# Kernel tuning notes

Measured on AMD Instinct MI355X. Metric: run time of the kernel, lower is better.

The kernel has to match this reference:

```python
import jax, jax.numpy as jnp
import numpy as np

N_NODES = 50000
N_EDGES = 800000
D = 64
N_GRAPHS = 500  # 100 nodes per graph


def setup_inputs() -> dict:
    key = jax.random.key(0)
    k1, k2, k3, k4, k5, k6 = jax.random.split(key, 6)
    x = jax.random.normal(k1, (N_NODES, D), dtype=jnp.float32)
    edge_index = jax.random.randint(k2, (2, N_EDGES), 0, N_NODES, dtype=jnp.int32)
    split_n = jnp.full((N_GRAPHS,), N_NODES // N_GRAPHS, dtype=jnp.int32)
    # edge_att_mlp: Linear(2*D, 1)
    W_edge = jax.random.normal(k3, (2 * D, 1), dtype=jnp.float32) * 0.05
    b_edge = jax.random.normal(k4, (1,), dtype=jnp.float32) * 0.05
    # node_att_cov: GCNConv(D, 1)
    W_gcn = jax.random.normal(k5, (D, 1), dtype=jnp.float32) * 0.05
    b_gcn = jax.random.normal(k6, (1,), dtype=jnp.float32) * 0.05
    return {"x": x, "edge_index": edge_index, "split_n": split_n,
            "W_edge": W_edge, "b_edge": b_edge, "W_gcn": W_gcn, "b_gcn": b_gcn}


def _segment_softmax(v, seg, num_segments):
    # softmax over dim 0 within each segment (replaces lazy_soft's python loop)
    m = jax.ops.segment_max(v, seg, num_segments=num_segments)
    e = jnp.exp(v - m[seg])
    s = jax.ops.segment_sum(e, seg, num_segments=num_segments)
    return e / s[seg]


def reference(x, edge_index, split_n, W_edge, b_edge, W_gcn, b_gcn):
    n = x.shape[0]
    row, col = edge_index[0], edge_index[1]

    # edge attention: gather pair, linear, sigmoid
    edge_rep = jnp.concatenate([x[row], x[col]], axis=-1)  # [E, 2D]
    edge_att = jax.nn.sigmoid(edge_rep @ W_edge + b_edge)  # [E, 1]
    edge_att_m = edge_att
    edge_att_s = 1.0 - edge_att

    # GCNConv(D, 1): add self-loops, symmetric deg^-1/2 norm, linear, scatter-sum
    h = x @ W_gcn  # [N, 1]
    loop = jnp.arange(n, dtype=row.dtype)
    src = jnp.concatenate([row, loop])
    dst = jnp.concatenate([col, loop])
    deg = jnp.zeros((n,), dtype=x.dtype).at[dst].add(1.0)
    dinv = jax.lax.rsqrt(deg)  # deg >= 1 due to self-loops
    norm = dinv[src] * dinv[dst]  # [E+N]
    node_att = jax.ops.segment_sum(norm[:, None] * h[src], dst, num_segments=n) + b_gcn

    # per-graph ragged softmax (fused segment softmax)
    seg = jnp.repeat(jnp.arange(split_n.shape[0]), split_n, total_repeat_length=n)
    node_att_m = _segment_softmax(node_att, seg, split_n.shape[0])
    node_att_s = _segment_softmax(1.0 - node_att_m, seg, split_n.shape[0])
    return edge_att_m, edge_att_s, node_att_m, node_att_s
```

## Files before the change

kernel.cpp:

```cpp
#include <hip/hip_runtime.h>
#include <math.h>


#define RANGE 8192
#define BD_H 1024
#define SOFT_LDS_CAP 2048

__global__ __launch_bounds__(BD_H)
void k1_node_hist(const float* __restrict__ x,
                  const float* __restrict__ W_edge,
                  const float* __restrict__ W_gcn,
                  const int* __restrict__ ei,
                  float2* __restrict__ ed2,
                  float* __restrict__ hbuf,
                  float* __restrict__ partial,
                  int N, int E, int C, int R, int CH, int nodeBlocks, int vec) {
    __shared__ float table[RANGE];
    const int bid = blockIdx.x, tid = threadIdx.x;
    if (bid < nodeBlocks) {
        float4* Wsh = (float4*)table;
        if (tid < 32) Wsh[tid] = ((const float4*)W_edge)[tid];
        else if (tid < 48) Wsh[tid] = ((const float4*)W_gcn)[tid - 32];
        __syncthreads();
        int lane = tid & 15;
        long long gid = (long long)bid * BD_H + tid;
        int i = (int)(gid >> 4);
        if (i >= N) return;
        float4 v = ((const float4*)(x + (size_t)i * 64))[lane];
        float4 wa = Wsh[lane], wb = Wsh[16 + lane], wg = Wsh[32 + lane];
        float p1 = v.x*wa.x + v.y*wa.y + v.z*wa.z + v.w*wa.w;
        float p2 = v.x*wb.x + v.y*wb.y + v.z*wb.z + v.w*wb.w;
        float p3 = v.x*wg.x + v.y*wg.y + v.z*wg.z + v.w*wg.w;
#pragma unroll
        for (int s = 1; s < 16; s <<= 1) {
            p1 += __shfl_xor(p1, s);
            p2 += __shfl_xor(p2, s);
            p3 += __shfl_xor(p3, s);
        }
        if (lane == 0) {
            ed2[i] = make_float2(p1, p2);
            hbuf[i] = p3;
        }
        return;
    }
    const int hb = bid - nodeBlocks;
    const int c = hb / R;
    const int r = hb - c * R;
    const int lo = r * RANGE;
    for (int j = tid; j < RANGE; j += BD_H) table[j] = 0.f;
    __syncthreads();
    const int e_lo = c * CH;
    const int e_hi = (E < e_lo + CH) ? E : (e_lo + CH);
    const int* __restrict__ col = ei + E;
    for (int e = e_lo + tid * 4; e < e_hi; e += BD_H * 4) {
        if (vec && e + 3 < e_hi) {
            int4 cc = *(const int4*)(col + e);
            unsigned u;
            u = (unsigned)(cc.x - lo); if (u < RANGE) atomicAdd(&table[u], 1.f);
            u = (unsigned)(cc.y - lo); if (u < RANGE) atomicAdd(&table[u], 1.f);
            u = (unsigned)(cc.z - lo); if (u < RANGE) atomicAdd(&table[u], 1.f);
            u = (unsigned)(cc.w - lo); if (u < RANGE) atomicAdd(&table[u], 1.f);
        } else {
            int ee = (e_hi < e + 4) ? e_hi : e + 4;
            for (int q = e; q < ee; ++q) {
                unsigned u = (unsigned)(col[q] - lo);
                if (u < RANGE) atomicAdd(&table[u], 1.f);
            }
        }
    }
    __syncthreads();
    const size_t base = (size_t)c * N;
    for (int j = tid; j < RANGE; j += BD_H) {
        int node = lo + j;
        if (node < N) partial[base + node] = table[j];
    }
}

__global__ __launch_bounds__(256)
void k2_dinv_sig(const int* __restrict__ ei,
                 const float2* __restrict__ ed2,
                 const float* __restrict__ b_edge,
                 const float* __restrict__ partial,
                 float* __restrict__ hbuf,
                 float* __restrict__ dv1,
                 float* __restrict__ om, float* __restrict__ os,
                 int N, int E, int C, int dinvBlocks, int vec) {
    const int bid = blockIdx.x, tid = threadIdx.x;
    if (bid < dinvBlocks) {
        int i = bid * 256 + tid;
        if (i >= N) return;
        float d0 = 1.f, d1 = 0.f, d2 = 0.f, d3 = 0.f;
        int c = 0;
        for (; c + 3 < C; c += 4) {
            d0 += partial[(size_t)(c + 0) * N + i];
            d1 += partial[(size_t)(c + 1) * N + i];
            d2 += partial[(size_t)(c + 2) * N + i];
            d3 += partial[(size_t)(c + 3) * N + i];
        }
        for (; c < C; ++c) d0 += partial[(size_t)c * N + i];
        float dv = rsqrtf((d0 + d1) + (d2 + d3));
        hbuf[i] *= dv;
        dv1[i] = dv;
        return;
    }
    int t = (bid - dinvBlocks) * 256 + tid;
    int e0 = t * 4;
    const float b = b_edge[0];
    if (vec && e0 + 3 < E) {
        int4 r = *(const int4*)(ei + e0);
        int4 c = *(const int4*)(ei + E + e0);
        float4 m;
        m.x = 1.f / (1.f + expf(-(ed2[r.x].x + ed2[c.x].y + b)));
        m.y = 1.f / (1.f + expf(-(ed2[r.y].x + ed2[c.y].y + b)));
        m.z = 1.f / (1.f + expf(-(ed2[r.z].x + ed2[c.z].y + b)));
        m.w = 1.f / (1.f + expf(-(ed2[r.w].x + ed2[c.w].y + b)));
        *(float4*)(om + e0) = m;
        *(float4*)(os + e0) = make_float4(1.f - m.x, 1.f - m.y, 1.f - m.z, 1.f - m.w);
    } else if (e0 < E) {
        int ee = (E < e0 + 4) ? E : e0 + 4;
        for (int e = e0; e < ee; ++e) {
            float a = 1.f / (1.f + expf(-(ed2[ei[e]].x + ed2[ei[E + e]].y + b)));
            om[e] = a; os[e] = 1.f - a;
        }
    }
}

__global__ __launch_bounds__(BD_H)
void k3_scat(const int* __restrict__ ei,
             const float* __restrict__ g1,
             float* __restrict__ partial,
             int N, int E, int C, int R, int CH, int vec) {
    __shared__ float table[RANGE];
    const int tid = threadIdx.x;
    const int c = blockIdx.x / R;
    const int r = blockIdx.x - c * R;
    const int lo = r * RANGE;
    for (int j = tid; j < RANGE; j += BD_H) table[j] = 0.f;
    __syncthreads();
    const int e_lo = c * CH;
    const int e_hi = (E < e_lo + CH) ? E : (e_lo + CH);
    const int* __restrict__ row = ei;
    const int* __restrict__ col = ei + E;
    for (int e = e_lo + tid * 4; e < e_hi; e += BD_H * 4) {
        if (vec && e + 3 < e_hi) {
            int4 cc = *(const int4*)(col + e);
            int4 rr = *(const int4*)(row + e);
            unsigned u;
            u = (unsigned)(cc.x - lo); if (u < RANGE) atomicAdd(&table[u], g1[rr.x]);
            u = (unsigned)(cc.y - lo); if (u < RANGE) atomicAdd(&table[u], g1[rr.y]);
            u = (unsigned)(cc.z - lo); if (u < RANGE) atomicAdd(&table[u], g1[rr.z]);
            u = (unsigned)(cc.w - lo); if (u < RANGE) atomicAdd(&table[u], g1[rr.w]);
        } else {
            int ee = (e_hi < e + 4) ? e_hi : e + 4;
            for (int q = e; q < ee; ++q) {
                unsigned u = (unsigned)(col[q] - lo);
                if (u < RANGE) atomicAdd(&table[u], g1[row[q]]);
            }
        }
    }
    __syncthreads();
    const size_t base = (size_t)c * N;
    for (int j = tid; j < RANGE; j += BD_H) {
        int node = lo + j;
        if (node < N) partial[base + node] = table[j];
    }
}

__global__ __launch_bounds__(128)
void k4_softmax(const float* __restrict__ hbuf,
                const float* __restrict__ dv1,
                const float* __restrict__ partial,
                float* __restrict__ accfb,
                const int* __restrict__ split_n,
                float* __restrict__ out_m, float* __restrict__ out_s,
                int N, int C) {
    __shared__ float red[128];
    __shared__ int ired[128];
    __shared__ int sh_off;
    __shared__ float sv[SOFT_LDS_CAP];
    const int g = blockIdx.x;
    const int tid = threadIdx.x;
    const int BD = blockDim.x;

    int part = 0;
    for (int j = tid; j < g; j += BD) part += split_n[j];
    ired[tid] = part; __syncthreads();
    for (int s = 64; s > 0; s >>= 1) {
        if (tid < s) ired[tid] += ired[tid + s];
        __syncthreads();
    }
    if (tid == 0) sh_off = ired[0];
    __syncthreads();
    const int off = sh_off;
    const int cnt = split_n[g];
    const bool fits = (cnt <= SOFT_LDS_CAP);

    for (int j = tid; j < cnt; j += BD) {
        int node = off + j;
        float s0 = hbuf[node], s1 = 0.f, s2 = 0.f, s3 = 0.f;
        int c = 0;
        for (; c + 3 < C; c += 4) {
            s0 += partial[(size_t)(c + 0) * N + node];
            s1 += partial[(size_t)(c + 1) * N + node];
            s2 += partial[(size_t)(c + 2) * N + node];
            s3 += partial[(size_t)(c + 3) * N + node];
        }
        for (; c < C; ++c) s0 += partial[(size_t)c * N + node];
        float a = dv1[node] * ((s0 + s1) + (s2 + s3));
        if (fits) sv[j] = a; else accfb[node] = a;
    }
    __syncthreads();

    float mx = -INFINITY;
    for (int j = tid; j < cnt; j += BD) mx = fmaxf(mx, fits ? sv[j] : accfb[off + j]);
    red[tid] = mx; __syncthreads();
    for (int s = 64; s > 0; s >>= 1) {
        if (tid < s) red[tid] = fmaxf(red[tid], red[tid + s]);
        __syncthreads();
    }
    mx = red[0]; __syncthreads();
    float sum = 0.f;
    for (int j = tid; j < cnt; j += BD) sum += expf((fits ? sv[j] : accfb[off + j]) - mx);
    red[tid] = sum; __syncthreads();
    for (int s = 64; s > 0; s >>= 1) {
        if (tid < s) red[tid] += red[tid + s];
        __syncthreads();
    }
    const float inv1 = 1.0f / red[0]; __syncthreads();
    for (int j = tid; j < cnt; j += BD) {
        float mv = expf((fits ? sv[j] : accfb[off + j]) - mx) * inv1;
        out_m[off + j] = mv;
        if (fits) sv[j] = mv;
    }
    __syncthreads();

    float mx2 = -INFINITY;
    for (int j = tid; j < cnt; j += BD)
        mx2 = fmaxf(mx2, 1.0f - (fits ? sv[j] : out_m[off + j]));
    red[tid] = mx2; __syncthreads();
    for (int s = 64; s > 0; s >>= 1) {
        if (tid < s) red[tid] = fmaxf(red[tid], red[tid + s]);
        __syncthreads();
    }
    mx2 = red[0]; __syncthreads();
    float sum2 = 0.f;
    for (int j = tid; j < cnt; j += BD)
        sum2 += expf(1.0f - (fits ? sv[j] : out_m[off + j]) - mx2);
    red[tid] = sum2; __syncthreads();
    for (int s = 64; s > 0; s >>= 1) {
        if (tid < s) red[tid] += red[tid + s];
        __syncthreads();
    }
    const float inv2 = 1.0f / red[0]; __syncthreads();
    for (int j = tid; j < cnt; j += BD)
        out_s[off + j] = expf(1.0f - (fits ? sv[j] : out_m[off + j]) - mx2) * inv2;
}

extern "C" void kernel_launch(void* const* d_in, const int* in_sizes, int n_in,
                              void* d_out, int out_size, void* d_ws, size_t ws_size,
                              hipStream_t stream) {
    const float* x      = (const float*)d_in[0];
    const int*   ei     = (const int*)d_in[1];
    const int*   splitn = (const int*)d_in[2];
    const float* W_edge = (const float*)d_in[3];
    const float* b_edge = (const float*)d_in[4];
    const float* W_gcn  = (const float*)d_in[5];

    const int N = in_sizes[0] / 64;
    const int E = in_sizes[1] / 2;
    const int G = in_sizes[2];

    float* out = (float*)d_out;
    float* edge_m = out;
    float* edge_s = out + E;
    float* node_m = out + 2LL * E;
    float* node_s = out + 2LL * E + N;

    int C = 64;
    while (C > 2 && (size_t)(5 + C) * N * sizeof(float) > ws_size) C >>= 1;
    const int R  = (N + RANGE - 1) / RANGE;
    const int CH = (((E + C - 1) / C) + 3) & ~3;
    const int vec = ((E & 3) == 0) ? 1 : 0;

    float2* ed2     = (float2*)d_ws;
    float*  hbuf    = (float*)d_ws + 2LL * N;
    float*  dv1     = hbuf + N;
    float*  accfb   = dv1 + N;
    float*  partial = accfb + N;

    const int nodeBlocks = (int)(((long long)N * 16 + BD_H - 1) / BD_H);
    const int dinvBlocks = (N + 255) / 256;
    const int sigBlocks  = ((E + 3) / 4 + 255) / 256;

    k1_node_hist<<<nodeBlocks + R * C, BD_H, 0, stream>>>(
        x, W_edge, W_gcn, ei, ed2, hbuf, partial, N, E, C, R, CH, nodeBlocks, vec);
    k2_dinv_sig<<<dinvBlocks + sigBlocks, 256, 0, stream>>>(
        ei, ed2, b_edge, partial, hbuf, dv1, edge_m, edge_s, N, E, C, dinvBlocks, vec);
    k3_scat<<<R * C, BD_H, 0, stream>>>(ei, hbuf, partial, N, E, C, R, CH, vec);
    k4_softmax<<<G, 128, 0, stream>>>(hbuf, dv1, partial, accfb, splitn,
                                      node_m, node_s, N, C);
}
```

Measured before the change: 56.00 us.

## Pack degree histogram into 16-bit LDS counters and split edge projection arrays

The degree histogram now packs two 16-bit counters per 32-bit shared-memory word, which doubles the node range covered per block (16384 instead of 8192). It also stores the per-chunk partial degrees as u16 instead of float. This cuts the number of histogram blocks that rescan the edge list and halves the partial-degree traffic read back in the dinv reduction. The float2 node projection array is split into two separate float arrays, so each edge gather loads 4 bytes instead of 8. A risk is 16-bit overflow if one chunk holds more than 65535 edges to a single node, which random inputs make unlikely.

```diff
diff --git a/kernel.cpp b/kernel.cpp
--- a/kernel.cpp
+++ b/kernel.cpp
@@ -2,23 +2,27 @@
 #include <math.h>
 
 
-#define RANGE 8192
+#define RANGE_S 8192
+#define RANGE_H 16384
 #define BD_H 1024
 #define SOFT_LDS_CAP 2048
+
+typedef unsigned short u16t;
+typedef unsigned int u32t;
 
 __global__ __launch_bounds__(BD_H)
 void k1_node_hist(const float* __restrict__ x,
                   const float* __restrict__ W_edge,
                   const float* __restrict__ W_gcn,
                   const int* __restrict__ ei,
-                  float2* __restrict__ ed2,
+                  float* __restrict__ pa, float* __restrict__ pb,
                   float* __restrict__ hbuf,
-                  float* __restrict__ partial,
-                  int N, int E, int C, int R, int CH, int nodeBlocks, int vec) {
-    __shared__ float table[RANGE];
+                  u16t* __restrict__ pd,
+                  int N, int E, int Ch, int Rh, int CHh, int nodeBlocks, int vec) {
+    __shared__ u32t t32[RANGE_H / 2];
     const int bid = blockIdx.x, tid = threadIdx.x;
     if (bid < nodeBlocks) {
-        float4* Wsh = (float4*)table;
+        float4* Wsh = (float4*)t32;
         if (tid < 32) Wsh[tid] = ((const float4*)W_edge)[tid];
         else if (tid < 48) Wsh[tid] = ((const float4*)W_gcn)[tid - 32];
         __syncthreads();
@@ -38,67 +42,69 @@
             p3 += __shfl_xor(p3, s);
         }
         if (lane == 0) {
-            ed2[i] = make_float2(p1, p2);
+            pa[i] = p1;
+            pb[i] = p2;
             hbuf[i] = p3;
         }
         return;
     }
     const int hb = bid - nodeBlocks;
-    const int c = hb / R;
-    const int r = hb - c * R;
-    const int lo = r * RANGE;
-    for (int j = tid; j < RANGE; j += BD_H) table[j] = 0.f;
-    __syncthreads();
-    const int e_lo = c * CH;
-    const int e_hi = (E < e_lo + CH) ? E : (e_lo + CH);
+    const int c = hb / Rh;
+    const int r = hb - c * Rh;
+    const int lo = r * RANGE_H;
+    for (int j = tid; j < RANGE_H / 2; j += BD_H) t32[j] = 0u;
+    __syncthreads();
+    const int e_lo = c * CHh;
+    const int e_hi = (E < e_lo + CHh) ? E : (e_lo + CHh);
     const int* __restrict__ col = ei + E;
     for (int e = e_lo + tid * 4; e < e_hi; e += BD_H * 4) {
         if (vec && e + 3 < e_hi) {
             int4 cc = *(const int4*)(col + e);
             unsigned u;
-            u = (unsigned)(cc.x - lo); if (u < RANGE) atomicAdd(&table[u], 1.f);
-            u = (unsigned)(cc.y - lo); if (u < RANGE) atomicAdd(&table[u], 1.f);
-            u = (unsigned)(cc.z - lo); if (u < RANGE) atomicAdd(&table[u], 1.f);
-            u = (unsigned)(cc.w - lo); if (u < RANGE) atomicAdd(&table[u], 1.f);
+            u = (unsigned)(cc.x - lo); if (u < RANGE_H) atomicAdd(&t32[u >> 1], 1u << ((u & 1) << 4));
+            u = (unsigned)(cc.y - lo); if (u < RANGE_H) atomicAdd(&t32[u >> 1], 1u << ((u & 1) << 4));
+            u = (unsigned)(cc.z - lo); if (u < RANGE_H) atomicAdd(&t32[u >> 1], 1u << ((u & 1) << 4));
+            u = (unsigned)(cc.w - lo); if (u < RANGE_H) atomicAdd(&t32[u >> 1], 1u << ((u & 1) << 4));
         } else {
             int ee = (e_hi < e + 4) ? e_hi : e + 4;
             for (int q = e; q < ee; ++q) {
                 unsigned u = (unsigned)(col[q] - lo);
-                if (u < RANGE) atomicAdd(&table[u], 1.f);
+                if (u < RANGE_H) atomicAdd(&t32[u >> 1], 1u << ((u & 1) << 4));
             }
         }
     }
     __syncthreads();
     const size_t base = (size_t)c * N;
-    for (int j = tid; j < RANGE; j += BD_H) {
+    for (int j = tid; j < RANGE_H; j += BD_H) {
         int node = lo + j;
-        if (node < N) partial[base + node] = table[j];
+        if (node < N)
+            pd[base + node] = (u16t)(t32[j >> 1] >> ((j & 1) << 4));
     }
 }
 
 __global__ __launch_bounds__(256)
 void k2_dinv_sig(const int* __restrict__ ei,
-                 const float2* __restrict__ ed2,
+                 const float* __restrict__ pa, const float* __restrict__ pb,
                  const float* __restrict__ b_edge,
-                 const float* __restrict__ partial,
+                 const u16t* __restrict__ pd,
                  float* __restrict__ hbuf,
                  float* __restrict__ dv1,
                  float* __restrict__ om, float* __restrict__ os,
-                 int N, int E, int C, int dinvBlocks, int vec) {
+                 int N, int E, int Ch, int dinvBlocks, int vec) {
     const int bid = blockIdx.x, tid = threadIdx.x;
     if (bid < dinvBlocks) {
         int i = bid * 256 + tid;
         if (i >= N) return;
-        float d0 = 1.f, d1 = 0.f, d2 = 0.f, d3 = 0.f;
+        unsigned d0 = 1u, d1 = 0u, d2 = 0u, d3 = 0u;
         int c = 0;
-        for (; c + 3 < C; c += 4) {
-            d0 += partial[(size_t)(c + 0) * N + i];
-            d1 += partial[(size_t)(c + 1) * N + i];
-            d2 += partial[(size_t)(c + 2) * N + i];
-            d3 += partial[(size_t)(c + 3) * N + i];
-        }
-        for (; c < C; ++c) d0 += partial[(size_t)c * N + i];
-        float dv = rsqrtf((d0 + d1) + (d2 + d3));
+        for (; c + 3 < Ch; c += 4) {
+            d0 += pd[(size_t)(c + 0) * N + i];
+            d1 += pd[(size_t)(c + 1) * N + i];
+            d2 += pd[(size_t)(c + 2) * N + i];
+            d3 += pd[(size_t)(c + 3) * N + i];
+        }
+        for (; c < Ch; ++c) d0 += pd[(size_t)c * N + i];
+        float dv = rsqrtf((float)((d0 + d1) + (d2 + d3)));
         hbuf[i] *= dv;
         dv1[i] = dv;
         return;
@@ -110,16 +116,16 @@
         int4 r = *(const int4*)(ei + e0);
         int4 c = *(const int4*)(ei + E + e0);
         float4 m;
-        m.x = 1.f / (1.f + expf(-(ed2[r.x].x + ed2[c.x].y + b)));
-        m.y = 1.f / (1.f + expf(-(ed2[r.y].x + ed2[c.y].y + b)));
-        m.z = 1.f / (1.f + expf(-(ed2[r.z].x + ed2[c.z].y + b)));
-        m.w = 1.f / (1.f + expf(-(ed2[r.w].x + ed2[c.w].y + b)));
+        m.x = 1.f / (1.f + expf(-(pa[r.x] + pb[c.x] + b)));
+        m.y = 1.f / (1.f + expf(-(pa[r.y] + pb[c.y] + b)));
+        m.z = 1.f / (1.f + expf(-(pa[r.z] + pb[c.z] + b)));
+        m.w = 1.f / (1.f + expf(-(pa[r.w] + pb[c.w] + b)));
         *(float4*)(om + e0) = m;
         *(float4*)(os + e0) = make_float4(1.f - m.x, 1.f - m.y, 1.f - m.z, 1.f - m.w);
     } else if (e0 < E) {
         int ee = (E < e0 + 4) ? E : e0 + 4;
         for (int e = e0; e < ee; ++e) {
-            float a = 1.f / (1.f + expf(-(ed2[ei[e]].x + ed2[ei[E + e]].y + b)));
+            float a = 1.f / (1.f + expf(-(pa[ei[e]] + pb[ei[E + e]] + b)));
             om[e] = a; os[e] = 1.f - a;
         }
     }
@@ -129,16 +135,16 @@
 void k3_scat(const int* __restrict__ ei,
              const float* __restrict__ g1,
              float* __restrict__ partial,
-             int N, int E, int C, int R, int CH, int vec) {
-    __shared__ float table[RANGE];
+             int N, int E, int Cs, int Rs, int CHs, int vec) {
+    __shared__ float table[RANGE_S];
     const int tid = threadIdx.x;
-    const int c = blockIdx.x / R;
-    const int r = blockIdx.x - c * R;
-    const int lo = r * RANGE;
-    for (int j = tid; j < RANGE; j += BD_H) table[j] = 0.f;
-    __syncthreads();
-    const int e_lo = c * CH;
-    const int e_hi = (E < e_lo + CH) ? E : (e_lo + CH);
+    const int c = blockIdx.x / Rs;
+    const int r = blockIdx.x - c * Rs;
+    const int lo = r * RANGE_S;
+    for (int j = tid; j < RANGE_S; j += BD_H) table[j] = 0.f;
+    __syncthreads();
+    const int e_lo = c * CHs;
+    const int e_hi = (E < e_lo + CHs) ? E : (e_lo + CHs);
     const int* __restrict__ row = ei;
     const int* __restrict__ col = ei + E;
     for (int e = e_lo + tid * 4; e < e_hi; e += BD_H * 4) {
@@ -146,21 +152,21 @@
             int4 cc = *(const int4*)(col + e);
             int4 rr = *(const int4*)(row + e);
             unsigned u;
-            u = (unsigned)(cc.x - lo); if (u < RANGE) atomicAdd(&table[u], g1[rr.x]);
-            u = (unsigned)(cc.y - lo); if (u < RANGE) atomicAdd(&table[u], g1[rr.y]);
-            u = (unsigned)(cc.z - lo); if (u < RANGE) atomicAdd(&table[u], g1[rr.z]);
-            u = (unsigned)(cc.w - lo); if (u < RANGE) atomicAdd(&table[u], g1[rr.w]);
+            u = (unsigned)(cc.x - lo); if (u < RANGE_S) atomicAdd(&table[u], g1[rr.x]);
+            u = (unsigned)(cc.y - lo); if (u < RANGE_S) atomicAdd(&table[u], g1[rr.y]);
+            u = (unsigned)(cc.z - lo); if (u < RANGE_S) atomicAdd(&table[u], g1[rr.z]);
+            u = (unsigned)(cc.w - lo); if (u < RANGE_S) atomicAdd(&table[u], g1[rr.w]);
         } else {
             int ee = (e_hi < e + 4) ? e_hi : e + 4;
             for (int q = e; q < ee; ++q) {
                 unsigned u = (unsigned)(col[q] - lo);
-                if (u < RANGE) atomicAdd(&table[u], g1[row[q]]);
+                if (u < RANGE_S) atomicAdd(&table[u], g1[row[q]]);
             }
         }
     }
     __syncthreads();
     const size_t base = (size_t)c * N;
-    for (int j = tid; j < RANGE; j += BD_H) {
+    for (int j = tid; j < RANGE_S; j += BD_H) {
         int node = lo + j;
         if (node < N) partial[base + node] = table[j];
     }
@@ -173,7 +179,7 @@
                 float* __restrict__ accfb,
                 const int* __restrict__ split_n,
                 float* __restrict__ out_m, float* __restrict__ out_s,
-                int N, int C) {
+                int N, int Cs) {
     __shared__ float red[128];
     __shared__ int ired[128];
     __shared__ int sh_off;
@@ -199,13 +205,13 @@
         int node = off + j;
         float s0 = hbuf[node], s1 = 0.f, s2 = 0.f, s3 = 0.f;
         int c = 0;
-        for (; c + 3 < C; c += 4) {
+        for (; c + 3 < Cs; c += 4) {
             s0 += partial[(size_t)(c + 0) * N + node];
             s1 += partial[(size_t)(c + 1) * N + node];
             s2 += partial[(size_t)(c + 2) * N + node];
             s3 += partial[(size_t)(c + 3) * N + node];
         }
-        for (; c < C; ++c) s0 += partial[(size_t)c * N + node];
+        for (; c < Cs; ++c) s0 += partial[(size_t)c * N + node];
         float a = dv1[node] * ((s0 + s1) + (s2 + s3));
         if (fits) sv[j] = a; else accfb[node] = a;
     }
@@ -276,27 +282,32 @@
     float* node_m = out + 2LL * E;
     float* node_s = out + 2LL * E + N;
 
-    int C = 64;
-    while (C > 2 && (size_t)(5 + C) * N * sizeof(float) > ws_size) C >>= 1;
-    const int R  = (N + RANGE - 1) / RANGE;
-    const int CH = (((E + C - 1) / C) + 3) & ~3;
+    int Cs = 64;
+    while (Cs > 2 && (size_t)(5 + Cs) * N * sizeof(float) > ws_size) Cs >>= 1;
+    const int Ch = Cs;
+    const int Rs = (N + RANGE_S - 1) / RANGE_S;
+    const int Rh = (N + RANGE_H - 1) / RANGE_H;
+    const int CHs = (((E + Cs - 1) / Cs) + 3) & ~3;
+    const int CHh = (((E + Ch - 1) / Ch) + 3) & ~3;
     const int vec = ((E & 3) == 0) ? 1 : 0;
 
-    float2* ed2     = (float2*)d_ws;
-    float*  hbuf    = (float*)d_ws + 2LL * N;
-    float*  dv1     = hbuf + N;
-    float*  accfb   = dv1 + N;
-    float*  partial = accfb + N;
+    float* pa      = (float*)d_ws;
+    float* pb      = pa + N;
+    float* hbuf    = pb + N;
+    float* dv1     = hbuf + N;
+    float* accfb   = dv1 + N;
+    float* partial = accfb + N;
+    u16t*  pd      = (u16t*)partial;
 
     const int nodeBlocks = (int)(((long long)N * 16 + BD_H - 1) / BD_H);
     const int dinvBlocks = (N + 255) / 256;
     const int sigBlocks  = ((E + 3) / 4 + 255) / 256;
 
-    k1_node_hist<<<nodeBlocks + R * C, BD_H, 0, stream>>>(
-        x, W_edge, W_gcn, ei, ed2, hbuf, partial, N, E, C, R, CH, nodeBlocks, vec);
+    k1_node_hist<<<nodeBlocks + Rh * Ch, BD_H, 0, stream>>>(
+        x, W_edge, W_gcn, ei, pa, pb, hbuf, pd, N, E, Ch, Rh, CHh, nodeBlocks, vec);
     k2_dinv_sig<<<dinvBlocks + sigBlocks, 256, 0, stream>>>(
-        ei, ed2, b_edge, partial, hbuf, dv1, edge_m, edge_s, N, E, C, dinvBlocks, vec);
-    k3_scat<<<R * C, BD_H, 0, stream>>>(ei, hbuf, partial, N, E, C, R, CH, vec);
+        ei, pa, pb, b_edge, pd, hbuf, dv1, edge_m, edge_s, N, E, Ch, dinvBlocks, vec);
+    k3_scat<<<Rs * Cs, BD_H, 0, stream>>>(ei, hbuf, partial, N, E, Cs, Rs, CHs, vec);
     k4_softmax<<<G, 128, 0, stream>>>(hbuf, dv1, partial, accfb, splitn,
-                                      node_m, node_s, N, C);
-}
+                                      node_m, node_s, N, Cs);
+}
```

After: 50.78 us. 9.3% less time.
